# Performance work log

Hardware: AMD Instinct MI355X
Metric: run time of the kernel (lower is better)

## Reference

```python
import jax, jax.numpy as jnp
import numpy as np

N_NODES = 50000
N_EDGES = 800000
DROP_P = 0.1


def setup_inputs() -> dict:
    key = jax.random.key(0)
    ks = jax.random.split(key, 8)
    x = jax.random.normal(ks[0], (N_NODES, 128), dtype=jnp.float32)
    edge_index = jax.random.randint(ks[1], (2, N_EDGES), 0, N_NODES, dtype=jnp.int64)
    # SAGEConv params: lin_l (applied to aggregated neighbors, has bias), lin_r (root, no bias)
    Wl1 = jax.random.normal(ks[2], (128, 256), dtype=jnp.float32) * 0.05
    Wr1 = jax.random.normal(ks[3], (128, 256), dtype=jnp.float32) * 0.05
    b1 = jax.random.normal(ks[4], (256,), dtype=jnp.float32) * 0.05
    Wl2 = jax.random.normal(ks[5], (256, 128), dtype=jnp.float32) * 0.05
    Wr2 = jax.random.normal(ks[6], (256, 128), dtype=jnp.float32) * 0.05
    b2 = jax.random.normal(ks[7], (128,), dtype=jnp.float32) * 0.05
    return {"x": x, "edge_index": edge_index, "Wl1": Wl1, "Wr1": Wr1, "b1": b1,
            "Wl2": Wl2, "Wr2": Wr2, "b2": b2}


def _sage_conv(x, src, dst, Wl, Wr, b, n_nodes):
    # PyG SAGEConv (mean aggr): out = lin_l(mean_{j in N(i)} x_j) + lin_r(x_i)
    msg = x[src]                                                  # [E, d] gather
    agg = jax.ops.segment_sum(msg, dst, num_segments=n_nodes)    # [N, d]
    cnt = jax.ops.segment_sum(jnp.ones((src.shape[0],), x.dtype), dst, num_segments=n_nodes)
    mean = agg / jnp.maximum(cnt, 1.0)[:, None]
    return mean @ Wl + x @ Wr + b


def reference(x, edge_index, Wl1, Wr1, b1, Wl2, Wr2, b2):
    src, dst = edge_index[0], edge_index[1]
    n = x.shape[0]
    h = _sage_conv(x, src, dst, Wl1, Wr1, b1, n)
    h = jax.nn.relu(h)
    # dropout p=0.1 with deterministic key (training=True in source)
    keep = jax.random.bernoulli(jax.random.key(42), 1.0 - DROP_P, h.shape)
    h = jnp.where(keep, h / (1.0 - DROP_P), 0.0)
    return _sage_conv(h, src, dst, Wl2, Wr2, b2, n)
```

## Files before the change

### kernel.cpp

```cpp
#include <hip/hip_runtime.h>

#define NN 50000
#define NE 800000
#define NBC 49
#define MSB 391

typedef __attribute__((ext_vector_type(8))) short short8;
typedef __attribute__((ext_vector_type(4))) float f32x4;

#define GLDS(g, l)                                                              \
  __builtin_amdgcn_global_load_lds(                                             \
      (const __attribute__((address_space(1))) void*)(g),                       \
      (__attribute__((address_space(3))) void*)(l), 16, 0, 0)

__device__ __forceinline__ unsigned short f2bf(float f) {
  union { float f; unsigned u; } v; v.f = f;
  unsigned r = (v.u + 0x7FFFu + ((v.u >> 16) & 1u)) >> 16;
  return (unsigned short)r;
}
__device__ __forceinline__ float bflo(unsigned u) {
  union { unsigned x; float f; } v; v.x = u << 16; return v.f;
}
__device__ __forceinline__ float bfhi(unsigned u) {
  union { unsigned x; float f; } v; v.x = u & 0xFFFF0000u; return v.f;
}

__device__ __forceinline__ unsigned tf_rotl(unsigned x, int r) {
#if __has_builtin(__builtin_amdgcn_alignbit)
  return __builtin_amdgcn_alignbit(x, x, 32 - r);
#else
  return (x << r) | (x >> (32 - r));
#endif
}
__device__ __forceinline__ void threefry_0_42(unsigned x0, unsigned x1,
                                              unsigned& o0, unsigned& o1) {
  const unsigned k0 = 0u, k1 = 42u;
  const unsigned k2 = k0 ^ k1 ^ 0x1BD11BDAu;
  x0 += k0; x1 += k1;
#define TF_R(r) { x0 += x1; x1 = tf_rotl(x1, (r)); x1 ^= x0; }
  TF_R(13) TF_R(15) TF_R(26) TF_R(6)
  x0 += k1; x1 += k2 + 1u;
  TF_R(17) TF_R(29) TF_R(16) TF_R(24)
  x0 += k2; x1 += k0 + 2u;
  TF_R(13) TF_R(15) TF_R(26) TF_R(6)
  x0 += k0; x1 += k1 + 3u;
  TF_R(17) TF_R(29) TF_R(16) TF_R(24)
  x0 += k1; x1 += k2 + 4u;
  TF_R(13) TF_R(15) TF_R(26) TF_R(6)
  x0 += k2; x1 += k0 + 5u;
#undef TF_R
  o0 = x0; o1 = x1;
}
__device__ __forceinline__ float dropout_scale(unsigned flat) {
  unsigned o0, o1;
  threefry_0_42(0u, flat, o0, o1);
  unsigned bits = o0 ^ o1;
  return ((bits >> 9) < 7549747u) ? (1.0f / 0.9f) : 0.0f;
}

__global__ void cvtx_k(const float4* __restrict__ x, uint2* __restrict__ xb, int n4) {
  int i = blockIdx.x * 256 + threadIdx.x;
  if (i >= n4) return;
  float4 v = x[i];
  uint2 o;
  o.x = (unsigned)f2bf(v.x) | ((unsigned)f2bf(v.y) << 16);
  o.y = (unsigned)f2bf(v.z) | ((unsigned)f2bf(v.w) << 16);
  xb[i] = o;
}

__global__ void mkw_k(const float* __restrict__ Wl1, const float* __restrict__ Wr1,
                      const float* __restrict__ Wl2, const float* __restrict__ Wr2,
                      unsigned short* __restrict__ W1t, unsigned short* __restrict__ W2t) {
  int gid = blockIdx.x * 256 + threadIdx.x;
  int idx = gid & 65535;
  int n = idx >> 8, k = idx & 255;
  if (gid < 65536) {
    float v = (k < 128) ? Wr1[(size_t)k * 256 + n] : Wl1[(size_t)(k - 128) * 256 + n];
    W1t[idx] = f2bf(v);
  } else {
    float v = (n < 128) ? Wl2[(size_t)k * 128 + n] : Wr2[(size_t)k * 128 + (n - 128)];
    W2t[idx] = f2bf(v);
  }
}

__global__ void zero4_k(float4* p, int n4) {
  int i = blockIdx.x * blockDim.x + threadIdx.x;
  if (i < n4) p[i] = make_float4(0.f, 0.f, 0.f, 0.f);
}

__global__ __launch_bounds__(256) void histC_k(const int* __restrict__ dst,
                                               unsigned* __restrict__ hist) {
  __shared__ unsigned lh[64];
  int tid = threadIdx.x;
  if (tid < 64) lh[tid] = 0;
  __syncthreads();
  int base = blockIdx.x * 2048;
#pragma unroll
  for (int k = 0; k < 8; ++k) {
    int e = base + k * 256 + tid;
    if (e < NE) atomicAdd(&lh[((unsigned)dst[e]) >> 10], 1u);
  }
  __syncthreads();
  if (tid < 64 && lh[tid]) atomicAdd(&hist[tid], lh[tid]);
}

__global__ __launch_bounds__(64) void scan64_k(const unsigned* __restrict__ hist,
                                               unsigned* __restrict__ bases,
                                               unsigned* __restrict__ gcur) {
  int tid = threadIdx.x;
  unsigned v = hist[tid], incl = v;
#pragma unroll
  for (int o = 1; o < 64; o <<= 1) {
    unsigned t = __shfl_up(incl, o);
    if (tid >= o) incl += t;
  }
  unsigned ex = incl - v;
  bases[tid] = ex;
  gcur[tid] = ex;
  if (tid == 63) bases[64] = incl;
}

__global__ __launch_bounds__(256) void msplit_k(const int* __restrict__ src,
                                                const int* __restrict__ dst,
                                                unsigned* __restrict__ gcur,
                                                unsigned* __restrict__ bufA) {
  __shared__ unsigned lh[64], gb[64], lc[64];
  int tid = threadIdx.x;
  if (tid < 64) { lh[tid] = 0; lc[tid] = 0; }
  __syncthreads();
  int base = blockIdx.x * 2048;
  unsigned s[8], d[8];
  bool val[8];
#pragma unroll
  for (int k = 0; k < 8; ++k) {
    int e = base + k * 256 + tid;
    val[k] = (e < NE);
    s[k] = val[k] ? (unsigned)src[e] : 0u;
    d[k] = val[k] ? (unsigned)dst[e] : 0u;
    if (val[k]) atomicAdd(&lh[d[k] >> 10], 1u);
  }
  __syncthreads();
  if (tid < 64 && lh[tid]) gb[tid] = atomicAdd(&gcur[tid], lh[tid]);
  __syncthreads();
#pragma unroll
  for (int k = 0; k < 8; ++k) {
    if (val[k]) {
      unsigned b = d[k] >> 10;
      unsigned pos = atomicAdd(&lc[b], 1u);
      bufA[gb[b] + pos] = (s[k] & 0xFFFFu) | ((d[k] & 1023u) << 16);
    }
  }
}

__global__ __launch_bounds__(1024) void passB2_k(const unsigned* __restrict__ bases,
                                                 const unsigned* __restrict__ bufA,
                                                 unsigned short* __restrict__ esrc,
                                                 unsigned* __restrict__ rowptr,
                                                 float* __restrict__ inv) {
  __shared__ unsigned cnt[1024], offs[1024], s_[1024];
  __shared__ unsigned short stage[18432];
  const int b = blockIdx.x, tid = threadIdx.x;
  const unsigned base0 = bases[b];
  const unsigned end0 = bases[b + 1];
  const unsigned bcnt = end0 - base0;

  cnt[tid] = 0;
  __syncthreads();
  for (unsigned i = tid; i < bcnt; i += 1024)
    atomicAdd(&cnt[bufA[base0 + i] >> 16], 1u);
  __syncthreads();

  unsigned c = cnt[tid];
  s_[tid] = c;
  __syncthreads();
  for (int o = 1; o < 1024; o <<= 1) {
    unsigned t = (tid >= o) ? s_[tid - o] : 0u;
    __syncthreads();
    s_[tid] += t;
    __syncthreads();
  }
  unsigned ex = s_[tid] - c;
  offs[tid] = ex;
  int node = b * 1024 + tid;
  if (node < NN) {
    rowptr[node] = base0 + ex;
    inv[node] = 1.0f / fmaxf((float)c, 1.0f);
  }
  cnt[tid] = 0;
  if (b == NBC - 1 && tid == 0) rowptr[NN] = NE;
  __syncthreads();

  if (bcnt <= 18432) {
    for (unsigned i = tid; i < bcnt; i += 1024) {
      unsigned w = bufA[base0 + i];
      unsigned dl = w >> 16;
      unsigned pos = atomicAdd(&cnt[dl], 1u);
      stage[offs[dl] + pos] = (unsigned short)w;
    }
    __syncthreads();
    for (unsigned i = tid; i < bcnt; i += 1024) esrc[base0 + i] = stage[i];
  } else {
    for (unsigned i = tid; i < bcnt; i += 1024) {
      unsigned w = bufA[base0 + i];
      unsigned dl = w >> 16;
      unsigned pos = atomicAdd(&cnt[dl], 1u);
      esrc[base0 + offs[dl] + pos] = (unsigned short)w;
    }
  }
}

__global__ __launch_bounds__(256) void gather_mean_k(
    const unsigned short* __restrict__ esrc, const unsigned* __restrict__ rowptr,
    const float* __restrict__ inv, const unsigned* __restrict__ xb,
    unsigned* __restrict__ meanb) {
  int node = blockIdx.x * 4 + (threadIdx.x >> 6);
  if (node >= NN) return;
  int lane = threadIdx.x & 63;
  unsigned beg = rowptr[node], end = rowptr[node + 1];
  float ax = 0.f, ay = 0.f;
  unsigned t = beg;
  for (; t + 4 <= end; t += 4) {
    unsigned s0 = esrc[t], s1 = esrc[t + 1], s2 = esrc[t + 2], s3 = esrc[t + 3];
    unsigned v0 = xb[(size_t)s0 * 64 + lane];
    unsigned v1 = xb[(size_t)s1 * 64 + lane];
    unsigned v2 = xb[(size_t)s2 * 64 + lane];
    unsigned v3 = xb[(size_t)s3 * 64 + lane];
    ax += (bflo(v0) + bflo(v1)) + (bflo(v2) + bflo(v3));
    ay += (bfhi(v0) + bfhi(v1)) + (bfhi(v2) + bfhi(v3));
  }
  for (; t < end; ++t) {
    unsigned v0 = xb[(size_t)esrc[t] * 64 + lane];
    ax += bflo(v0); ay += bfhi(v0);
  }
  float sc = inv[node];
  meanb[(size_t)node * 64 + lane] =
      (unsigned)f2bf(ax * sc) | ((unsigned)f2bf(ay * sc) << 16);
}

__global__ __launch_bounds__(256) void gather_add_k(
    const unsigned short* __restrict__ esrc, const unsigned* __restrict__ rowptr,
    const float* __restrict__ inv, const unsigned* __restrict__ P,
    float* __restrict__ out) {
  int node = blockIdx.x * 4 + (threadIdx.x >> 6);
  if (node >= NN) return;
  int lane = threadIdx.x & 63;
  unsigned beg = rowptr[node], end = rowptr[node + 1];
  float ax = 0.f, ay = 0.f;
  unsigned t = beg;
  for (; t + 4 <= end; t += 4) {
    unsigned s0 = esrc[t], s1 = esrc[t + 1], s2 = esrc[t + 2], s3 = esrc[t + 3];
    unsigned v0 = P[(size_t)s0 * 64 + lane];
    unsigned v1 = P[(size_t)s1 * 64 + lane];
    unsigned v2 = P[(size_t)s2 * 64 + lane];
    unsigned v3 = P[(size_t)s3 * 64 + lane];
    ax += (bflo(v0) + bflo(v1)) + (bflo(v2) + bflo(v3));
    ay += (bfhi(v0) + bfhi(v1)) + (bfhi(v2) + bfhi(v3));
  }
  for (; t < end; ++t) {
    unsigned v0 = P[(size_t)esrc[t] * 64 + lane];
    ax += bflo(v0); ay += bfhi(v0);
  }
  float sc = inv[node];
  float2* O = (float2*)out;
  float2 o = O[(size_t)node * 64 + lane];
  o.x += ax * sc;
  o.y += ay * sc;
  O[(size_t)node * 64 + lane] = o;
}


__global__ __launch_bounds__(256) void mgemm1_k(
    const unsigned short* __restrict__ xb, const unsigned short* __restrict__ meanb,
    const unsigned short* __restrict__ W1t, const float* __restrict__ b1,
    unsigned short* __restrict__ h) {
  __shared__ __align__(16) char As[64 * 64 * 2];
  __shared__ __align__(16) char Bs[64 * 64 * 2];
  const int tid = threadIdx.x;
  const int lane = tid & 63, wid = tid >> 6;
  const int wm = (wid >> 1) * 32, wn = (wid & 1) * 32;
  const int r16 = lane & 15, g = lane >> 4;
  const unsigned bid = blockIdx.x;
  const unsigned v_ = (bid & 7u) * 391u + (bid >> 3);
  const int m0 = (int)(v_ >> 2) * 64;
  const int j0 = (int)(v_ & 3u) * 64;
  const int wbase = (tid & ~63);

  const unsigned short* aSrcX[2];
  const unsigned short* aSrcM[2];
  const unsigned short* bSrc[2];
  char* ldsA[2];
  char* ldsB[2];
#pragma unroll
  for (int p = 0; p < 2; ++p) {
    int id = p * 256 + tid;
    int r = id >> 3, cb = id & 7;
    int grow = m0 + r;
    if (grow >= NN) grow = NN - 1;
    int swz = (cb ^ (r & 7)) << 3;
    aSrcX[p] = xb + (size_t)grow * 128 + swz;
    aSrcM[p] = meanb + (size_t)grow * 128 + swz;
    bSrc[p] = W1t + (size_t)(j0 + r) * 256 + swz;
    ldsA[p] = As + ((p * 256 + wbase) << 4);
    ldsB[p] = Bs + ((p * 256 + wbase) << 4);
  }

  int aoff[2][2], boff[2][2];
#pragma unroll
  for (int f = 0; f < 2; ++f)
#pragma unroll
    for (int ks = 0; ks < 2; ++ks) {
      int ar = wm + f * 16 + r16;
      aoff[f][ks] = ar * 128 + ((ks * 64 + g * 16) ^ ((ar & 7) << 4));
      int br = wn + f * 16 + r16;
      boff[f][ks] = br * 128 + ((ks * 64 + g * 16) ^ ((br & 7) << 4));
    }

  f32x4 acc[2][2] = {};

  auto compute = [&]() {
#pragma unroll
    for (int ks = 0; ks < 2; ++ks) {
      short8 af[2], bf[2];
#pragma unroll
      for (int f = 0; f < 2; ++f) {
        af[f] = *(const short8*)(As + aoff[f][ks]);
        bf[f] = *(const short8*)(Bs + boff[f][ks]);
      }
#pragma unroll
      for (int i = 0; i < 2; ++i)
#pragma unroll
        for (int j = 0; j < 2; ++j)
          acc[i][j] = __builtin_amdgcn_mfma_f32_16x16x32_bf16(af[i], bf[j], acc[i][j], 0, 0, 0);
    }
  };

  GLDS(aSrcX[0], ldsA[0]); GLDS(aSrcX[1], ldsA[1]);
  GLDS(bSrc[0], ldsB[0]);  GLDS(bSrc[1], ldsB[1]);

  float dsc[2][2][4];
#pragma unroll
  for (int i = 0; i < 2; ++i)
#pragma unroll
    for (int j = 0; j < 2; ++j) {
      int col = j0 + wn + j * 16 + r16;
#pragma unroll
      for (int q = 0; q < 4; ++q) {
        int row = m0 + wm + i * 16 + g * 4 + q;
        dsc[i][j][q] = dropout_scale((unsigned)row * 256u + (unsigned)col);
      }
    }

  __syncthreads();
  compute();
  __syncthreads();
  GLDS(aSrcX[0] + 64, ldsA[0]); GLDS(aSrcX[1] + 64, ldsA[1]);
  GLDS(bSrc[0] + 64, ldsB[0]);  GLDS(bSrc[1] + 64, ldsB[1]);
  __syncthreads();
  compute();
  __syncthreads();
  GLDS(aSrcM[0], ldsA[0]);       GLDS(aSrcM[1], ldsA[1]);
  GLDS(bSrc[0] + 128, ldsB[0]);  GLDS(bSrc[1] + 128, ldsB[1]);
  __syncthreads();
  compute();
  __syncthreads();
  GLDS(aSrcM[0] + 64, ldsA[0]);  GLDS(aSrcM[1] + 64, ldsA[1]);
  GLDS(bSrc[0] + 192, ldsB[0]);  GLDS(bSrc[1] + 192, ldsB[1]);
  __syncthreads();
  compute();

#pragma unroll
  for (int i = 0; i < 2; ++i)
#pragma unroll
    for (int j = 0; j < 2; ++j) {
      int col = j0 + wn + j * 16 + r16;
      float bias = b1[col];
#pragma unroll
      for (int q = 0; q < 4; ++q) {
        int row = m0 + wm + i * 16 + g * 4 + q;
        if (row < NN) {
          float v = fmaxf(acc[i][j][q] + bias, 0.f) * dsc[i][j][q];
          h[(size_t)row * 256 + col] = f2bf(v);
        }
      }
    }
}

__global__ __launch_bounds__(256) void mgemm2_k(
    const unsigned short* __restrict__ h, const unsigned short* __restrict__ W2t,
    const float* __restrict__ b2, unsigned short* __restrict__ P,
    float* __restrict__ out) {
  __shared__ __align__(16) char As[64 * 64 * 2];
  __shared__ __align__(16) char Bs[64 * 64 * 2];
  const int tid = threadIdx.x;
  const int lane = tid & 63, wid = tid >> 6;
  const int wm = (wid >> 1) * 32, wn = (wid & 1) * 32;
  const int r16 = lane & 15, g = lane >> 4;
  const unsigned bid = blockIdx.x;
  const unsigned v_ = (bid & 7u) * 391u + (bid >> 3);
  const int m0 = (int)(v_ >> 2) * 64;
  const int j0 = (int)(v_ & 3u) * 64;
  const int wbase = (tid & ~63);

  const unsigned short* aSrc[2];
  const unsigned short* bSrc[2];
  char* ldsA[2];
  char* ldsB[2];
#pragma unroll
  for (int p = 0; p < 2; ++p) {
    int id = p * 256 + tid;
    int r = id >> 3, cb = id & 7;
    int grow = m0 + r;
    if (grow >= NN) grow = NN - 1;
    int swz = (cb ^ (r & 7)) << 3;
    aSrc[p] = h + (size_t)grow * 256 + swz;
    bSrc[p] = W2t + (size_t)(j0 + r) * 256 + swz;
    ldsA[p] = As + ((p * 256 + wbase) << 4);
    ldsB[p] = Bs + ((p * 256 + wbase) << 4);
  }

  int aoff[2][2], boff[2][2];
#pragma unroll
  for (int f = 0; f < 2; ++f)
#pragma unroll
    for (int ks = 0; ks < 2; ++ks) {
      int ar = wm + f * 16 + r16;
      aoff[f][ks] = ar * 128 + ((ks * 64 + g * 16) ^ ((ar & 7) << 4));
      int br = wn + f * 16 + r16;
      boff[f][ks] = br * 128 + ((ks * 64 + g * 16) ^ ((br & 7) << 4));
    }

  f32x4 acc[2][2] = {};

  auto compute = [&]() {
#pragma unroll
    for (int ks = 0; ks < 2; ++ks) {
      short8 af[2], bf[2];
#pragma unroll
      for (int f = 0; f < 2; ++f) {
        af[f] = *(const short8*)(As + aoff[f][ks]);
        bf[f] = *(const short8*)(Bs + boff[f][ks]);
      }
#pragma unroll
      for (int i = 0; i < 2; ++i)
#pragma unroll
        for (int j = 0; j < 2; ++j)
          acc[i][j] = __builtin_amdgcn_mfma_f32_16x16x32_bf16(af[i], bf[j], acc[i][j], 0, 0, 0);
    }
  };

  GLDS(aSrc[0], ldsA[0]); GLDS(aSrc[1], ldsA[1]);
  GLDS(bSrc[0], ldsB[0]); GLDS(bSrc[1], ldsB[1]);
  __syncthreads();
  compute();
  __syncthreads();
  GLDS(aSrc[0] + 64, ldsA[0]); GLDS(aSrc[1] + 64, ldsA[1]);
  GLDS(bSrc[0] + 64, ldsB[0]); GLDS(bSrc[1] + 64, ldsB[1]);
  __syncthreads();
  compute();
  __syncthreads();
  GLDS(aSrc[0] + 128, ldsA[0]); GLDS(aSrc[1] + 128, ldsA[1]);
  GLDS(bSrc[0] + 128, ldsB[0]); GLDS(bSrc[1] + 128, ldsB[1]);
  __syncthreads();
  compute();
  __syncthreads();
  GLDS(aSrc[0] + 192, ldsA[0]); GLDS(aSrc[1] + 192, ldsA[1]);
  GLDS(bSrc[0] + 192, ldsB[0]); GLDS(bSrc[1] + 192, ldsB[1]);
  __syncthreads();
  compute();

#pragma unroll
  for (int i = 0; i < 2; ++i)
#pragma unroll
    for (int j = 0; j < 2; ++j) {
      int col = j0 + wn + j * 16 + r16;
#pragma unroll
      for (int q = 0; q < 4; ++q) {
        int row = m0 + wm + i * 16 + g * 4 + q;
        if (row < NN) {
          if (col < 128) {
            P[(size_t)row * 128 + col] = f2bf(acc[i][j][q]);
          } else {
            out[(size_t)row * 128 + (col - 128)] = acc[i][j][q] + b2[col - 128];
          }
        }
      }
    }
}

extern "C" void kernel_launch(void* const* d_in, const int* in_sizes, int n_in,
                              void* d_out, int out_size, void* d_ws, size_t ws_size,
                              hipStream_t stream) {
  const float* x   = (const float*)d_in[0];
  const int*   ei  = (const int*)d_in[1];
  const float* Wl1 = (const float*)d_in[2];
  const float* Wr1 = (const float*)d_in[3];
  const float* b1  = (const float*)d_in[4];
  const float* Wl2 = (const float*)d_in[5];
  const float* Wr2 = (const float*)d_in[6];
  const float* b2  = (const float*)d_in[7];
  float* out = (float*)d_out;

  const int* src = ei;
  const int* dst = ei + NE;

  char* ws = (char*)d_ws;
  unsigned*       rowptr = (unsigned*)ws;
  float*          inv    = (float*)(ws + 0x40000);
  unsigned*       hist   = (unsigned*)(ws + 0x80000);
  unsigned*       bases  = (unsigned*)(ws + 0x80400);
  unsigned*       gcur   = (unsigned*)(ws + 0x80800);
  unsigned short* esrc   = (unsigned short*)(ws + 0xC0000);
  unsigned*       bufA   = (unsigned*)(ws + 0x280000);
  unsigned short* W1t    = (unsigned short*)(ws + 0x600000);
  unsigned short* W2t    = (unsigned short*)(ws + 0x620000);
  unsigned short* xb     = (unsigned short*)(ws + 0x700000);
  unsigned short* meanb  = (unsigned short*)(ws + 0x1400000);
  unsigned short* h      = (unsigned short*)(ws + 0x2100000);
  unsigned short* P      = (unsigned short*)(ws + 0x3A00000);

  const int TPB = 256;

  cvtx_k<<<(NN * 128 / 4 + TPB - 1) / TPB, TPB, 0, stream>>>((const float4*)x, (uint2*)xb, NN * 128 / 4);
  mkw_k<<<512, TPB, 0, stream>>>(Wl1, Wr1, Wl2, Wr2, W1t, W2t);

  zero4_k<<<1, TPB, 0, stream>>>((float4*)hist, 16);
  histC_k<<<MSB, TPB, 0, stream>>>(dst, hist);
  scan64_k<<<1, 64, 0, stream>>>(hist, bases, gcur);
  msplit_k<<<MSB, TPB, 0, stream>>>(src, dst, gcur, bufA);
  passB2_k<<<NBC, 1024, 0, stream>>>(bases, bufA, esrc, rowptr, inv);

  gather_mean_k<<<(NN + 3) / 4, TPB, 0, stream>>>(esrc, rowptr, inv, (const unsigned*)xb, (unsigned*)meanb);
  mgemm1_k<<<3128, TPB, 0, stream>>>(xb, meanb, W1t, b1, h);

  mgemm2_k<<<3128, TPB, 0, stream>>>(h, W2t, b2, P, out);
  gather_add_k<<<(NN + 3) / 4, TPB, 0, stream>>>(esrc, rowptr, inv, (const unsigned*)P, out);
}
```

Measured before the change: 184.2 us.

## Double-buffer GEMM LDS tiles, merge prep kernels, widen gather unroll

```diff
diff --git a/kernel.cpp b/kernel.cpp
--- a/kernel.cpp
+++ b/kernel.cpp
@@ -3,7 +3,7 @@
 #define NN 50000
 #define NE 800000
 #define NBC 49
-#define MSB 391
+#define MSB 782
 
 typedef __attribute__((ext_vector_type(8))) short short8;
 typedef __attribute__((ext_vector_type(4))) float f32x4;
@@ -58,34 +58,31 @@
   return ((bits >> 9) < 7549747u) ? (1.0f / 0.9f) : 0.0f;
 }
 
-__global__ void cvtx_k(const float4* __restrict__ x, uint2* __restrict__ xb, int n4) {
-  int i = blockIdx.x * 256 + threadIdx.x;
-  if (i >= n4) return;
-  float4 v = x[i];
-  uint2 o;
-  o.x = (unsigned)f2bf(v.x) | ((unsigned)f2bf(v.y) << 16);
-  o.y = (unsigned)f2bf(v.z) | ((unsigned)f2bf(v.w) << 16);
-  xb[i] = o;
-}
-
-__global__ void mkw_k(const float* __restrict__ Wl1, const float* __restrict__ Wr1,
-                      const float* __restrict__ Wl2, const float* __restrict__ Wr2,
-                      unsigned short* __restrict__ W1t, unsigned short* __restrict__ W2t) {
-  int gid = blockIdx.x * 256 + threadIdx.x;
-  int idx = gid & 65535;
-  int n = idx >> 8, k = idx & 255;
-  if (gid < 65536) {
-    float v = (k < 128) ? Wr1[(size_t)k * 256 + n] : Wl1[(size_t)(k - 128) * 256 + n];
-    W1t[idx] = f2bf(v);
+#define CVTB 6250
+__global__ void prep_k(const float4* __restrict__ x, uint2* __restrict__ xb,
+                       const float* __restrict__ Wl1, const float* __restrict__ Wr1,
+                       const float* __restrict__ Wl2, const float* __restrict__ Wr2,
+                       unsigned short* __restrict__ W1t, unsigned short* __restrict__ W2t) {
+  int bid = blockIdx.x;
+  if (bid < CVTB) {
+    int i = bid * 256 + threadIdx.x;
+    float4 v = x[i];
+    uint2 o;
+    o.x = (unsigned)f2bf(v.x) | ((unsigned)f2bf(v.y) << 16);
+    o.y = (unsigned)f2bf(v.z) | ((unsigned)f2bf(v.w) << 16);
+    xb[i] = o;
   } else {
-    float v = (n < 128) ? Wl2[(size_t)k * 128 + n] : Wr2[(size_t)k * 128 + (n - 128)];
-    W2t[idx] = f2bf(v);
-  }
-}
-
-__global__ void zero4_k(float4* p, int n4) {
-  int i = blockIdx.x * blockDim.x + threadIdx.x;
-  if (i < n4) p[i] = make_float4(0.f, 0.f, 0.f, 0.f);
+    int gid = (bid - CVTB) * 256 + threadIdx.x;
+    int idx = gid & 65535;
+    int n = idx >> 8, k = idx & 255;
+    if (gid < 65536) {
+      float v = (k < 128) ? Wr1[(size_t)k * 256 + n] : Wl1[(size_t)(k - 128) * 256 + n];
+      W1t[idx] = f2bf(v);
+    } else {
+      float v = (n < 128) ? Wl2[(size_t)k * 128 + n] : Wr2[(size_t)k * 128 + (n - 128)];
+      W2t[idx] = f2bf(v);
+    }
+  }
 }
 
 __global__ __launch_bounds__(256) void histC_k(const int* __restrict__ dst,
@@ -94,9 +91,9 @@
   int tid = threadIdx.x;
   if (tid < 64) lh[tid] = 0;
   __syncthreads();
-  int base = blockIdx.x * 2048;
-#pragma unroll
-  for (int k = 0; k < 8; ++k) {
+  int base = blockIdx.x * 1024;
+#pragma unroll
+  for (int k = 0; k < 4; ++k) {
     int e = base + k * 256 + tid;
     if (e < NE) atomicAdd(&lh[((unsigned)dst[e]) >> 10], 1u);
   }
@@ -128,11 +125,11 @@
   int tid = threadIdx.x;
   if (tid < 64) { lh[tid] = 0; lc[tid] = 0; }
   __syncthreads();
-  int base = blockIdx.x * 2048;
-  unsigned s[8], d[8];
-  bool val[8];
-#pragma unroll
-  for (int k = 0; k < 8; ++k) {
+  int base = blockIdx.x * 1024;
+  unsigned s[4], d[4];
+  bool val[4];
+#pragma unroll
+  for (int k = 0; k < 4; ++k) {
     int e = base + k * 256 + tid;
     val[k] = (e < NE);
     s[k] = val[k] ? (unsigned)src[e] : 0u;
@@ -143,7 +140,7 @@
   if (tid < 64 && lh[tid]) gb[tid] = atomicAdd(&gcur[tid], lh[tid]);
   __syncthreads();
 #pragma unroll
-  for (int k = 0; k < 8; ++k) {
+  for (int k = 0; k < 4; ++k) {
     if (val[k]) {
       unsigned b = d[k] >> 10;
       unsigned pos = atomicAdd(&lc[b], 1u);
@@ -219,12 +216,25 @@
   unsigned beg = rowptr[node], end = rowptr[node + 1];
   float ax = 0.f, ay = 0.f;
   unsigned t = beg;
+  for (; t + 8 <= end; t += 8) {
+    unsigned v0 = xb[(size_t)esrc[t + 0] * 64 + lane];
+    unsigned v1 = xb[(size_t)esrc[t + 1] * 64 + lane];
+    unsigned v2 = xb[(size_t)esrc[t + 2] * 64 + lane];
+    unsigned v3 = xb[(size_t)esrc[t + 3] * 64 + lane];
+    unsigned v4 = xb[(size_t)esrc[t + 4] * 64 + lane];
+    unsigned v5 = xb[(size_t)esrc[t + 5] * 64 + lane];
+    unsigned v6 = xb[(size_t)esrc[t + 6] * 64 + lane];
+    unsigned v7 = xb[(size_t)esrc[t + 7] * 64 + lane];
+    ax += ((bflo(v0) + bflo(v1)) + (bflo(v2) + bflo(v3))) +
+          ((bflo(v4) + bflo(v5)) + (bflo(v6) + bflo(v7)));
+    ay += ((bfhi(v0) + bfhi(v1)) + (bfhi(v2) + bfhi(v3))) +
+          ((bfhi(v4) + bfhi(v5)) + (bfhi(v6) + bfhi(v7)));
+  }
   for (; t + 4 <= end; t += 4) {
-    unsigned s0 = esrc[t], s1 = esrc[t + 1], s2 = esrc[t + 2], s3 = esrc[t + 3];
-    unsigned v0 = xb[(size_t)s0 * 64 + lane];
-    unsigned v1 = xb[(size_t)s1 * 64 + lane];
-    unsigned v2 = xb[(size_t)s2 * 64 + lane];
-    unsigned v3 = xb[(size_t)s3 * 64 + lane];
+    unsigned v0 = xb[(size_t)esrc[t + 0] * 64 + lane];
+    unsigned v1 = xb[(size_t)esrc[t + 1] * 64 + lane];
+    unsigned v2 = xb[(size_t)esrc[t + 2] * 64 + lane];
+    unsigned v3 = xb[(size_t)esrc[t + 3] * 64 + lane];
     ax += (bflo(v0) + bflo(v1)) + (bflo(v2) + bflo(v3));
     ay += (bfhi(v0) + bfhi(v1)) + (bfhi(v2) + bfhi(v3));
   }
@@ -247,12 +257,25 @@
   unsigned beg = rowptr[node], end = rowptr[node + 1];
   float ax = 0.f, ay = 0.f;
   unsigned t = beg;
+  for (; t + 8 <= end; t += 8) {
+    unsigned v0 = P[(size_t)esrc[t + 0] * 64 + lane];
+    unsigned v1 = P[(size_t)esrc[t + 1] * 64 + lane];
+    unsigned v2 = P[(size_t)esrc[t + 2] * 64 + lane];
+    unsigned v3 = P[(size_t)esrc[t + 3] * 64 + lane];
+    unsigned v4 = P[(size_t)esrc[t + 4] * 64 + lane];
+    unsigned v5 = P[(size_t)esrc[t + 5] * 64 + lane];
+    unsigned v6 = P[(size_t)esrc[t + 6] * 64 + lane];
+    unsigned v7 = P[(size_t)esrc[t + 7] * 64 + lane];
+    ax += ((bflo(v0) + bflo(v1)) + (bflo(v2) + bflo(v3))) +
+          ((bflo(v4) + bflo(v5)) + (bflo(v6) + bflo(v7)));
+    ay += ((bfhi(v0) + bfhi(v1)) + (bfhi(v2) + bfhi(v3))) +
+          ((bfhi(v4) + bfhi(v5)) + (bfhi(v6) + bfhi(v7)));
+  }
   for (; t + 4 <= end; t += 4) {
-    unsigned s0 = esrc[t], s1 = esrc[t + 1], s2 = esrc[t + 2], s3 = esrc[t + 3];
-    unsigned v0 = P[(size_t)s0 * 64 + lane];
-    unsigned v1 = P[(size_t)s1 * 64 + lane];
-    unsigned v2 = P[(size_t)s2 * 64 + lane];
-    unsigned v3 = P[(size_t)s3 * 64 + lane];
+    unsigned v0 = P[(size_t)esrc[t + 0] * 64 + lane];
+    unsigned v1 = P[(size_t)esrc[t + 1] * 64 + lane];
+    unsigned v2 = P[(size_t)esrc[t + 2] * 64 + lane];
+    unsigned v3 = P[(size_t)esrc[t + 3] * 64 + lane];
     ax += (bflo(v0) + bflo(v1)) + (bflo(v2) + bflo(v3));
     ay += (bfhi(v0) + bfhi(v1)) + (bfhi(v2) + bfhi(v3));
   }
@@ -273,8 +296,8 @@
     const unsigned short* __restrict__ xb, const unsigned short* __restrict__ meanb,
     const unsigned short* __restrict__ W1t, const float* __restrict__ b1,
     unsigned short* __restrict__ h) {
-  __shared__ __align__(16) char As[64 * 64 * 2];
-  __shared__ __align__(16) char Bs[64 * 64 * 2];
+  __shared__ __align__(16) char As[2 * 8192];
+  __shared__ __align__(16) char Bs[2 * 8192];
   const int tid = threadIdx.x;
   const int lane = tid & 63, wid = tid >> 6;
   const int wm = (wid >> 1) * 32, wn = (wid & 1) * 32;
@@ -288,8 +311,8 @@
   const unsigned short* aSrcX[2];
   const unsigned short* aSrcM[2];
   const unsigned short* bSrc[2];
-  char* ldsA[2];
-  char* ldsB[2];
+  char* ldsA[2][2];
+  char* ldsB[2][2];
 #pragma unroll
   for (int p = 0; p < 2; ++p) {
     int id = p * 256 + tid;
@@ -300,8 +323,10 @@
     aSrcX[p] = xb + (size_t)grow * 128 + swz;
     aSrcM[p] = meanb + (size_t)grow * 128 + swz;
     bSrc[p] = W1t + (size_t)(j0 + r) * 256 + swz;
-    ldsA[p] = As + ((p * 256 + wbase) << 4);
-    ldsB[p] = Bs + ((p * 256 + wbase) << 4);
+    ldsA[0][p] = As + ((p * 256 + wbase) << 4);
+    ldsA[1][p] = ldsA[0][p] + 8192;
+    ldsB[0][p] = Bs + ((p * 256 + wbase) << 4);
+    ldsB[1][p] = ldsB[0][p] + 8192;
   }
 
   int aoff[2][2], boff[2][2];
@@ -317,14 +342,14 @@
 
   f32x4 acc[2][2] = {};
 
-  auto compute = [&]() {
+  auto compute = [&](const char* Ab, const char* Bb) {
 #pragma unroll
     for (int ks = 0; ks < 2; ++ks) {
       short8 af[2], bf[2];
 #pragma unroll
       for (int f = 0; f < 2; ++f) {
-        af[f] = *(const short8*)(As + aoff[f][ks]);
-        bf[f] = *(const short8*)(Bs + boff[f][ks]);
+        af[f] = *(const short8*)(Ab + aoff[f][ks]);
+        bf[f] = *(const short8*)(Bb + boff[f][ks]);
       }
 #pragma unroll
       for (int i = 0; i < 2; ++i)
@@ -334,8 +359,8 @@
     }
   };
 
-  GLDS(aSrcX[0], ldsA[0]); GLDS(aSrcX[1], ldsA[1]);
-  GLDS(bSrc[0], ldsB[0]);  GLDS(bSrc[1], ldsB[1]);
+  GLDS(aSrcX[0], ldsA[0][0]); GLDS(aSrcX[1], ldsA[0][1]);
+  GLDS(bSrc[0],  ldsB[0][0]); GLDS(bSrc[1],  ldsB[0][1]);
 
   float dsc[2][2][4];
 #pragma unroll
@@ -351,22 +376,19 @@
     }
 
   __syncthreads();
-  compute();
-  __syncthreads();
-  GLDS(aSrcX[0] + 64, ldsA[0]); GLDS(aSrcX[1] + 64, ldsA[1]);
-  GLDS(bSrc[0] + 64, ldsB[0]);  GLDS(bSrc[1] + 64, ldsB[1]);
-  __syncthreads();
-  compute();
-  __syncthreads();
-  GLDS(aSrcM[0], ldsA[0]);       GLDS(aSrcM[1], ldsA[1]);
-  GLDS(bSrc[0] + 128, ldsB[0]);  GLDS(bSrc[1] + 128, ldsB[1]);
-  __syncthreads();
-  compute();
-  __syncthreads();
-  GLDS(aSrcM[0] + 64, ldsA[0]);  GLDS(aSrcM[1] + 64, ldsA[1]);
-  GLDS(bSrc[0] + 192, ldsB[0]);  GLDS(bSrc[1] + 192, ldsB[1]);
-  __syncthreads();
-  compute();
+  GLDS(aSrcX[0] + 64, ldsA[1][0]); GLDS(aSrcX[1] + 64, ldsA[1][1]);
+  GLDS(bSrc[0] + 64,  ldsB[1][0]); GLDS(bSrc[1] + 64,  ldsB[1][1]);
+  compute(As, Bs);
+  __syncthreads();
+  GLDS(aSrcM[0], ldsA[0][0]);      GLDS(aSrcM[1], ldsA[0][1]);
+  GLDS(bSrc[0] + 128, ldsB[0][0]); GLDS(bSrc[1] + 128, ldsB[0][1]);
+  compute(As + 8192, Bs + 8192);
+  __syncthreads();
+  GLDS(aSrcM[0] + 64, ldsA[1][0]); GLDS(aSrcM[1] + 64, ldsA[1][1]);
+  GLDS(bSrc[0] + 192, ldsB[1][0]); GLDS(bSrc[1] + 192, ldsB[1][1]);
+  compute(As, Bs);
+  __syncthreads();
+  compute(As + 8192, Bs + 8192);
 
 #pragma unroll
   for (int i = 0; i < 2; ++i)
@@ -389,8 +411,8 @@
     const unsigned short* __restrict__ h, const unsigned short* __restrict__ W2t,
     const float* __restrict__ b2, unsigned short* __restrict__ P,
     float* __restrict__ out) {
-  __shared__ __align__(16) char As[64 * 64 * 2];
-  __shared__ __align__(16) char Bs[64 * 64 * 2];
+  __shared__ __align__(16) char As[2 * 8192];
+  __shared__ __align__(16) char Bs[2 * 8192];
   const int tid = threadIdx.x;
   const int lane = tid & 63, wid = tid >> 6;
   const int wm = (wid >> 1) * 32, wn = (wid & 1) * 32;
@@ -403,8 +425,8 @@
 
   const unsigned short* aSrc[2];
   const unsigned short* bSrc[2];
-  char* ldsA[2];
-  char* ldsB[2];
+  char* ldsA[2][2];
+  char* ldsB[2][2];
 #pragma unroll
   for (int p = 0; p < 2; ++p) {
     int id = p * 256 + tid;
@@ -414,8 +436,10 @@
     int swz = (cb ^ (r & 7)) << 3;
     aSrc[p] = h + (size_t)grow * 256 + swz;
     bSrc[p] = W2t + (size_t)(j0 + r) * 256 + swz;
-    ldsA[p] = As + ((p * 256 + wbase) << 4);
-    ldsB[p] = Bs + ((p * 256 + wbase) << 4);
+    ldsA[0][p] = As + ((p * 256 + wbase) << 4);
+    ldsA[1][p] = ldsA[0][p] + 8192;
+    ldsB[0][p] = Bs + ((p * 256 + wbase) << 4);
+    ldsB[1][p] = ldsB[0][p] + 8192;
   }
 
   int aoff[2][2], boff[2][2];
@@ -431,14 +455,14 @@
 
   f32x4 acc[2][2] = {};
 
-  auto compute = [&]() {
+  auto compute = [&](const char* Ab, const char* Bb) {
 #pragma unroll
     for (int ks = 0; ks < 2; ++ks) {
       short8 af[2], bf[2];
 #pragma unroll
       for (int f = 0; f < 2; ++f) {
-        af[f] = *(const short8*)(As + aoff[f][ks]);
-        bf[f] = *(const short8*)(Bs + boff[f][ks]);
+        af[f] = *(const short8*)(Ab + aoff[f][ks]);
+        bf[f] = *(const short8*)(Bb + boff[f][ks]);
       }
 #pragma unroll
       for (int i = 0; i < 2; ++i)
@@ -448,25 +472,22 @@
     }
   };
 
-  GLDS(aSrc[0], ldsA[0]); GLDS(aSrc[1], ldsA[1]);
-  GLDS(bSrc[0], ldsB[0]); GLDS(bSrc[1], ldsB[1]);
-  __syncthreads();
-  compute();
-  __syncthreads();
-  GLDS(aSrc[0] + 64, ldsA[0]); GLDS(aSrc[1] + 64, ldsA[1]);
-  GLDS(bSrc[0] + 64, ldsB[0]); GLDS(bSrc[1] + 64, ldsB[1]);
-  __syncthreads();
-  compute();
-  __syncthreads();
-  GLDS(aSrc[0] + 128, ldsA[0]); GLDS(aSrc[1] + 128, ldsA[1]);
-  GLDS(bSrc[0] + 128, ldsB[0]); GLDS(bSrc[1] + 128, ldsB[1]);
-  __syncthreads();
-  compute();
-  __syncthreads();
-  GLDS(aSrc[0] + 192, ldsA[0]); GLDS(aSrc[1] + 192, ldsA[1]);
-  GLDS(bSrc[0] + 192, ldsB[0]); GLDS(bSrc[1] + 192, ldsB[1]);
-  __syncthreads();
-  compute();
+  GLDS(aSrc[0], ldsA[0][0]); GLDS(aSrc[1], ldsA[0][1]);
+  GLDS(bSrc[0], ldsB[0][0]); GLDS(bSrc[1], ldsB[0][1]);
+  __syncthreads();
+  GLDS(aSrc[0] + 64, ldsA[1][0]); GLDS(aSrc[1] + 64, ldsA[1][1]);
+  GLDS(bSrc[0] + 64, ldsB[1][0]); GLDS(bSrc[1] + 64, ldsB[1][1]);
+  compute(As, Bs);
+  __syncthreads();
+  GLDS(aSrc[0] + 128, ldsA[0][0]); GLDS(aSrc[1] + 128, ldsA[0][1]);
+  GLDS(bSrc[0] + 128, ldsB[0][0]); GLDS(bSrc[1] + 128, ldsB[0][1]);
+  compute(As + 8192, Bs + 8192);
+  __syncthreads();
+  GLDS(aSrc[0] + 192, ldsA[1][0]); GLDS(aSrc[1] + 192, ldsA[1][1]);
+  GLDS(bSrc[0] + 192, ldsB[1][0]); GLDS(bSrc[1] + 192, ldsB[1][1]);
+  compute(As, Bs);
+  __syncthreads();
+  compute(As + 8192, Bs + 8192);
 
 #pragma unroll
   for (int i = 0; i < 2; ++i)
@@ -520,10 +541,10 @@
 
   const int TPB = 256;
 
-  cvtx_k<<<(NN * 128 / 4 + TPB - 1) / TPB, TPB, 0, stream>>>((const float4*)x, (uint2*)xb, NN * 128 / 4);
-  mkw_k<<<512, TPB, 0, stream>>>(Wl1, Wr1, Wl2, Wr2, W1t, W2t);
-
-  zero4_k<<<1, TPB, 0, stream>>>((float4*)hist, 16);
+  prep_k<<<CVTB + 512, TPB, 0, stream>>>((const float4*)x, (uint2*)xb,
+                                         Wl1, Wr1, Wl2, Wr2, W1t, W2t);
+  hipMemsetAsync(hist, 0, 64 * sizeof(unsigned), stream);
+
   histC_k<<<MSB, TPB, 0, stream>>>(dst, hist);
   scan64_k<<<1, 64, 0, stream>>>(hist, bases, gcur);
   msplit_k<<<MSB, TPB, 0, stream>>>(src, dst, gcur, bufA);
```

New measurement: 190.6 us. 1.03x slower.

## Precompute dropout bitmask in fused prep kernel, unroll gathers, split edge blocks

Applied to the files above, without the earlier changes.

```diff
diff --git a/kernel.cpp b/kernel.cpp
--- a/kernel.cpp
+++ b/kernel.cpp
@@ -3,7 +3,7 @@
 #define NN 50000
 #define NE 800000
 #define NBC 49
-#define MSB 391
+#define MSB 782
 
 typedef __attribute__((ext_vector_type(8))) short short8;
 typedef __attribute__((ext_vector_type(4))) float f32x4;
@@ -51,41 +51,50 @@
 #undef TF_R
   o0 = x0; o1 = x1;
 }
-__device__ __forceinline__ float dropout_scale(unsigned flat) {
-  unsigned o0, o1;
-  threefry_0_42(0u, flat, o0, o1);
-  unsigned bits = o0 ^ o1;
-  return ((bits >> 9) < 7549747u) ? (1.0f / 0.9f) : 0.0f;
-}
-
-__global__ void cvtx_k(const float4* __restrict__ x, uint2* __restrict__ xb, int n4) {
-  int i = blockIdx.x * 256 + threadIdx.x;
-  if (i >= n4) return;
-  float4 v = x[i];
-  uint2 o;
-  o.x = (unsigned)f2bf(v.x) | ((unsigned)f2bf(v.y) << 16);
-  o.y = (unsigned)f2bf(v.z) | ((unsigned)f2bf(v.w) << 16);
-  xb[i] = o;
-}
-
-__global__ void mkw_k(const float* __restrict__ Wl1, const float* __restrict__ Wr1,
-                      const float* __restrict__ Wl2, const float* __restrict__ Wr2,
-                      unsigned short* __restrict__ W1t, unsigned short* __restrict__ W2t) {
-  int gid = blockIdx.x * 256 + threadIdx.x;
-  int idx = gid & 65535;
-  int n = idx >> 8, k = idx & 255;
-  if (gid < 65536) {
-    float v = (k < 128) ? Wr1[(size_t)k * 256 + n] : Wl1[(size_t)(k - 128) * 256 + n];
-    W1t[idx] = f2bf(v);
+
+#define CVTB 6250
+#define MSKW 400000
+#define MSKB 1563
+__global__ void prep_k(const float4* __restrict__ x, uint2* __restrict__ xb,
+                       const float* __restrict__ Wl1, const float* __restrict__ Wr1,
+                       const float* __restrict__ Wl2, const float* __restrict__ Wr2,
+                       unsigned short* __restrict__ W1t, unsigned short* __restrict__ W2t,
+                       unsigned* __restrict__ msk, unsigned* __restrict__ hist) {
+  int bid = blockIdx.x;
+  if (bid < CVTB) {
+    int i = bid * 256 + threadIdx.x;
+    float4 v = x[i];
+    uint2 o;
+    o.x = (unsigned)f2bf(v.x) | ((unsigned)f2bf(v.y) << 16);
+    o.y = (unsigned)f2bf(v.z) | ((unsigned)f2bf(v.w) << 16);
+    xb[i] = o;
+  } else if (bid < CVTB + 512) {
+    int gid = (bid - CVTB) * 256 + threadIdx.x;
+    int idx = gid & 65535;
+    int n = idx >> 8, k = idx & 255;
+    if (gid < 65536) {
+      float v = (k < 128) ? Wr1[(size_t)k * 256 + n] : Wl1[(size_t)(k - 128) * 256 + n];
+      W1t[idx] = f2bf(v);
+    } else {
+      float v = (n < 128) ? Wl2[(size_t)k * 128 + n] : Wr2[(size_t)k * 128 + (n - 128)];
+      W2t[idx] = f2bf(v);
+    }
+  } else if (bid < CVTB + 512 + MSKB) {
+    int w = (bid - CVTB - 512) * 256 + threadIdx.x;
+    if (w < MSKW) {
+      unsigned base = (unsigned)w * 32u;
+      unsigned m = 0;
+#pragma unroll
+      for (int b = 0; b < 32; ++b) {
+        unsigned o0, o1;
+        threefry_0_42(0u, base + (unsigned)b, o0, o1);
+        if (((o0 ^ o1) >> 9) < 7549747u) m |= (1u << b);
+      }
+      msk[w] = m;
+    }
   } else {
-    float v = (n < 128) ? Wl2[(size_t)k * 128 + n] : Wr2[(size_t)k * 128 + (n - 128)];
-    W2t[idx] = f2bf(v);
-  }
-}
-
-__global__ void zero4_k(float4* p, int n4) {
-  int i = blockIdx.x * blockDim.x + threadIdx.x;
-  if (i < n4) p[i] = make_float4(0.f, 0.f, 0.f, 0.f);
+    if (threadIdx.x < 64) hist[threadIdx.x] = 0;
+  }
 }
 
 __global__ __launch_bounds__(256) void histC_k(const int* __restrict__ dst,
@@ -94,9 +103,9 @@
   int tid = threadIdx.x;
   if (tid < 64) lh[tid] = 0;
   __syncthreads();
-  int base = blockIdx.x * 2048;
-#pragma unroll
-  for (int k = 0; k < 8; ++k) {
+  int base = blockIdx.x * 1024;
+#pragma unroll
+  for (int k = 0; k < 4; ++k) {
     int e = base + k * 256 + tid;
     if (e < NE) atomicAdd(&lh[((unsigned)dst[e]) >> 10], 1u);
   }
@@ -128,11 +137,11 @@
   int tid = threadIdx.x;
   if (tid < 64) { lh[tid] = 0; lc[tid] = 0; }
   __syncthreads();
-  int base = blockIdx.x * 2048;
-  unsigned s[8], d[8];
-  bool val[8];
-#pragma unroll
-  for (int k = 0; k < 8; ++k) {
+  int base = blockIdx.x * 1024;
+  unsigned s[4], d[4];
+  bool val[4];
+#pragma unroll
+  for (int k = 0; k < 4; ++k) {
     int e = base + k * 256 + tid;
     val[k] = (e < NE);
     s[k] = val[k] ? (unsigned)src[e] : 0u;
@@ -143,7 +152,7 @@
   if (tid < 64 && lh[tid]) gb[tid] = atomicAdd(&gcur[tid], lh[tid]);
   __syncthreads();
 #pragma unroll
-  for (int k = 0; k < 8; ++k) {
+  for (int k = 0; k < 4; ++k) {
     if (val[k]) {
       unsigned b = d[k] >> 10;
       unsigned pos = atomicAdd(&lc[b], 1u);
@@ -219,12 +228,25 @@
   unsigned beg = rowptr[node], end = rowptr[node + 1];
   float ax = 0.f, ay = 0.f;
   unsigned t = beg;
+  for (; t + 8 <= end; t += 8) {
+    unsigned v0 = xb[(size_t)esrc[t + 0] * 64 + lane];
+    unsigned v1 = xb[(size_t)esrc[t + 1] * 64 + lane];
+    unsigned v2 = xb[(size_t)esrc[t + 2] * 64 + lane];
+    unsigned v3 = xb[(size_t)esrc[t + 3] * 64 + lane];
+    unsigned v4 = xb[(size_t)esrc[t + 4] * 64 + lane];
+    unsigned v5 = xb[(size_t)esrc[t + 5] * 64 + lane];
+    unsigned v6 = xb[(size_t)esrc[t + 6] * 64 + lane];
+    unsigned v7 = xb[(size_t)esrc[t + 7] * 64 + lane];
+    ax += ((bflo(v0) + bflo(v1)) + (bflo(v2) + bflo(v3))) +
+          ((bflo(v4) + bflo(v5)) + (bflo(v6) + bflo(v7)));
+    ay += ((bfhi(v0) + bfhi(v1)) + (bfhi(v2) + bfhi(v3))) +
+          ((bfhi(v4) + bfhi(v5)) + (bfhi(v6) + bfhi(v7)));
+  }
   for (; t + 4 <= end; t += 4) {
-    unsigned s0 = esrc[t], s1 = esrc[t + 1], s2 = esrc[t + 2], s3 = esrc[t + 3];
-    unsigned v0 = xb[(size_t)s0 * 64 + lane];
-    unsigned v1 = xb[(size_t)s1 * 64 + lane];
-    unsigned v2 = xb[(size_t)s2 * 64 + lane];
-    unsigned v3 = xb[(size_t)s3 * 64 + lane];
+    unsigned v0 = xb[(size_t)esrc[t + 0] * 64 + lane];
+    unsigned v1 = xb[(size_t)esrc[t + 1] * 64 + lane];
+    unsigned v2 = xb[(size_t)esrc[t + 2] * 64 + lane];
+    unsigned v3 = xb[(size_t)esrc[t + 3] * 64 + lane];
     ax += (bflo(v0) + bflo(v1)) + (bflo(v2) + bflo(v3));
     ay += (bfhi(v0) + bfhi(v1)) + (bfhi(v2) + bfhi(v3));
   }
@@ -247,12 +269,25 @@
   unsigned beg = rowptr[node], end = rowptr[node + 1];
   float ax = 0.f, ay = 0.f;
   unsigned t = beg;
+  for (; t + 8 <= end; t += 8) {
+    unsigned v0 = P[(size_t)esrc[t + 0] * 64 + lane];
+    unsigned v1 = P[(size_t)esrc[t + 1] * 64 + lane];
+    unsigned v2 = P[(size_t)esrc[t + 2] * 64 + lane];
+    unsigned v3 = P[(size_t)esrc[t + 3] * 64 + lane];
+    unsigned v4 = P[(size_t)esrc[t + 4] * 64 + lane];
+    unsigned v5 = P[(size_t)esrc[t + 5] * 64 + lane];
+    unsigned v6 = P[(size_t)esrc[t + 6] * 64 + lane];
+    unsigned v7 = P[(size_t)esrc[t + 7] * 64 + lane];
+    ax += ((bflo(v0) + bflo(v1)) + (bflo(v2) + bflo(v3))) +
+          ((bflo(v4) + bflo(v5)) + (bflo(v6) + bflo(v7)));
+    ay += ((bfhi(v0) + bfhi(v1)) + (bfhi(v2) + bfhi(v3))) +
+          ((bfhi(v4) + bfhi(v5)) + (bfhi(v6) + bfhi(v7)));
+  }
   for (; t + 4 <= end; t += 4) {
-    unsigned s0 = esrc[t], s1 = esrc[t + 1], s2 = esrc[t + 2], s3 = esrc[t + 3];
-    unsigned v0 = P[(size_t)s0 * 64 + lane];
-    unsigned v1 = P[(size_t)s1 * 64 + lane];
-    unsigned v2 = P[(size_t)s2 * 64 + lane];
-    unsigned v3 = P[(size_t)s3 * 64 + lane];
+    unsigned v0 = P[(size_t)esrc[t + 0] * 64 + lane];
+    unsigned v1 = P[(size_t)esrc[t + 1] * 64 + lane];
+    unsigned v2 = P[(size_t)esrc[t + 2] * 64 + lane];
+    unsigned v3 = P[(size_t)esrc[t + 3] * 64 + lane];
     ax += (bflo(v0) + bflo(v1)) + (bflo(v2) + bflo(v3));
     ay += (bfhi(v0) + bfhi(v1)) + (bfhi(v2) + bfhi(v3));
   }
@@ -272,7 +307,7 @@
 __global__ __launch_bounds__(256) void mgemm1_k(
     const unsigned short* __restrict__ xb, const unsigned short* __restrict__ meanb,
     const unsigned short* __restrict__ W1t, const float* __restrict__ b1,
-    unsigned short* __restrict__ h) {
+    const unsigned* __restrict__ msk, unsigned short* __restrict__ h) {
   __shared__ __align__(16) char As[64 * 64 * 2];
   __shared__ __align__(16) char Bs[64 * 64 * 2];
   const int tid = threadIdx.x;
@@ -336,20 +371,6 @@
 
   GLDS(aSrcX[0], ldsA[0]); GLDS(aSrcX[1], ldsA[1]);
   GLDS(bSrc[0], ldsB[0]);  GLDS(bSrc[1], ldsB[1]);
-
-  float dsc[2][2][4];
-#pragma unroll
-  for (int i = 0; i < 2; ++i)
-#pragma unroll
-    for (int j = 0; j < 2; ++j) {
-      int col = j0 + wn + j * 16 + r16;
-#pragma unroll
-      for (int q = 0; q < 4; ++q) {
-        int row = m0 + wm + i * 16 + g * 4 + q;
-        dsc[i][j][q] = dropout_scale((unsigned)row * 256u + (unsigned)col);
-      }
-    }
-
   __syncthreads();
   compute();
   __syncthreads();
@@ -378,7 +399,9 @@
       for (int q = 0; q < 4; ++q) {
         int row = m0 + wm + i * 16 + g * 4 + q;
         if (row < NN) {
-          float v = fmaxf(acc[i][j][q] + bias, 0.f) * dsc[i][j][q];
+          unsigned flat = (unsigned)row * 256u + (unsigned)col;
+          unsigned keep = (msk[flat >> 5] >> (flat & 31u)) & 1u;
+          float v = fmaxf(acc[i][j][q] + bias, 0.f) * (keep ? (1.0f / 0.9f) : 0.f);
           h[(size_t)row * 256 + col] = f2bf(v);
         }
       }
@@ -517,20 +540,20 @@
   unsigned short* meanb  = (unsigned short*)(ws + 0x1400000);
   unsigned short* h      = (unsigned short*)(ws + 0x2100000);
   unsigned short* P      = (unsigned short*)(ws + 0x3A00000);
+  unsigned*       msk    = (unsigned*)(ws + 0x3A00000);
 
   const int TPB = 256;
 
-  cvtx_k<<<(NN * 128 / 4 + TPB - 1) / TPB, TPB, 0, stream>>>((const float4*)x, (uint2*)xb, NN * 128 / 4);
-  mkw_k<<<512, TPB, 0, stream>>>(Wl1, Wr1, Wl2, Wr2, W1t, W2t);
-
-  zero4_k<<<1, TPB, 0, stream>>>((float4*)hist, 16);
+  prep_k<<<CVTB + 512 + MSKB + 1, TPB, 0, stream>>>(
+      (const float4*)x, (uint2*)xb, Wl1, Wr1, Wl2, Wr2, W1t, W2t, msk, hist);
+
   histC_k<<<MSB, TPB, 0, stream>>>(dst, hist);
   scan64_k<<<1, 64, 0, stream>>>(hist, bases, gcur);
   msplit_k<<<MSB, TPB, 0, stream>>>(src, dst, gcur, bufA);
   passB2_k<<<NBC, 1024, 0, stream>>>(bases, bufA, esrc, rowptr, inv);
 
   gather_mean_k<<<(NN + 3) / 4, TPB, 0, stream>>>(esrc, rowptr, inv, (const unsigned*)xb, (unsigned*)meanb);
-  mgemm1_k<<<3128, TPB, 0, stream>>>(xb, meanb, W1t, b1, h);
+  mgemm1_k<<<3128, TPB, 0, stream>>>(xb, meanb, W1t, b1, msk, h);
 
   mgemm2_k<<<3128, TPB, 0, stream>>>(h, W2t, b2, P, out);
   gather_add_k<<<(NN + 3) / 4, TPB, 0, stream>>>(esrc, rowptr, inv, (const unsigned*)P, out);
```

Result: slower. 196.6 us (+6.7%).
